# Kernel tuning notes

Measured on AMD Instinct MI355X. Metric: run time of the kernel, lower is better.

## Reference

```python
import jax, jax.numpy as jnp
import numpy as np

N_USERS = 100000
N_ITEMS = 100000
D = 64
B = 2048


def _ancf_layer(q, keys, aW, ab, W1, W2):
    # AttentionMechanism: hidden = relu(keys @ aW.T + ab)  [N, d]
    hidden = jax.nn.relu(keys @ aW.T + ab)
    # scores [B, N]; softmax over keys (dim=1)
    attn = jax.nn.softmax(q @ hidden.T, axis=1)
    q2 = q + attn @ keys  # [B, d]
    # MessageAggregation loop collapsed algebraically:
    # out = W1(q2) + sum_j W1(k_j) + sum_j W2(q2 * k_j)
    #     = W1(q2) + W1(S) + W2(q2 * S),  S = sum_j k_j
    S = keys.sum(axis=0)  # [d]
    out = (q2 + S) @ W1.T + (q2 * S) @ W2.T
    return jax.nn.leaky_relu(out, 0.01)


def setup_inputs() -> dict:
    key = jax.random.key(0)
    ks = jax.random.split(key, 12)
    scale_emb = 0.1
    scale_w = (2.0 / (D + D)) ** 0.5  # xavier-normal std for square layers
    inp = {
        "user_emb": jax.random.normal(ks[0], (N_USERS, D), jnp.float32) * scale_emb,
        "item_emb": jax.random.normal(ks[1], (N_ITEMS, D), jnp.float32) * scale_emb,
        "u_attn_W": jax.random.normal(ks[2], (D, D), jnp.float32) * scale_w,
        "u_attn_b": jnp.zeros((D,), jnp.float32),
        "u_W1": jax.random.normal(ks[3], (D, D), jnp.float32) * scale_w,
        "u_W2": jax.random.normal(ks[4], (D, D), jnp.float32) * scale_w,
        "i_attn_W": jax.random.normal(ks[5], (D, D), jnp.float32) * scale_w,
        "i_attn_b": jnp.zeros((D,), jnp.float32),
        "i_W1": jax.random.normal(ks[6], (D, D), jnp.float32) * scale_w,
        "i_W2": jax.random.normal(ks[7], (D, D), jnp.float32) * scale_w,
        "user_id": jax.random.randint(ks[8], (B,), 0, N_USERS),
        "item_id": jax.random.randint(ks[9], (B,), 0, N_ITEMS),
        "all_user_ids": jnp.arange(N_USERS),
        "all_item_ids": jnp.arange(N_ITEMS),
    }
    return inp


def reference(user_emb, item_emb, u_attn_W, u_attn_b, u_W1, u_W2,
              i_attn_W, i_attn_b, i_W1, i_W2,
              user_id, item_id, all_user_ids, all_item_ids):
    all_user_embeddings = user_emb[all_user_ids]  # [N_users, d]
    all_item_embeddings = item_emb[all_item_ids]  # [N_items, d]
    ue = all_user_embeddings[user_id]  # [B, d]
    ie = all_item_embeddings[item_id]  # [B, d]

    ue_out = _ancf_layer(ue, all_item_embeddings, u_attn_W, u_attn_b, u_W1, u_W2)
    ie_out = _ancf_layer(ie, all_user_embeddings, i_attn_W, i_attn_b, i_W1, i_W2)

    og_user = jnp.concatenate([ue, ue_out], axis=1)  # [B, 2d]
    og_item = jnp.concatenate([ie, ie_out], axis=1)  # [B, 2d]
    return og_user.T @ og_item  # [2d, 2d]
```

## Files before the change

kernel.cpp:

```cpp
#include <hip/hip_runtime.h>


typedef __bf16 bf16x8 __attribute__((ext_vector_type(8)));
typedef float f32x2 __attribute__((ext_vector_type(2)));
typedef float f32x4 __attribute__((ext_vector_type(4)));
typedef float f32x16 __attribute__((ext_vector_type(16)));
typedef unsigned int u32x4 __attribute__((ext_vector_type(4)));
typedef int i32x4 __attribute__((ext_vector_type(4)));
typedef int i32x8 __attribute__((ext_vector_type(8)));

static constexpr int NKEYS  = 100000;
static constexpr int NP     = 101376;
static constexpr int DIM    = 64;
static constexpr int BQ     = 2048;
static constexpr int NCH    = 48;
static constexpr int CHROWS = NP / NCH;
static constexpr int NPH    = CHROWS / 64;
static constexpr int NTIL   = NP / 64;
static constexpr float PADCNT = float(NP - NKEYS);
static constexpr float LOG2E  = 1.44269504088896340736f;

#define DEVINL __device__ __forceinline__

DEVINL unsigned int cvtpk(float lo, float hi) {
    unsigned int r;
    asm("v_cvt_pk_bf16_f32 %0, %1, %2" : "=v"(r) : "v"(lo), "v"(hi));
    return r;
}
DEVINL unsigned short bfr(float f) {
    return (unsigned short)(cvtpk(f, f) & 0xffffu);
}
DEVINL float bf2f(unsigned short u) {
    unsigned int w = (unsigned int)u << 16;
    return __builtin_bit_cast(float, w);
}
DEVINL void permswap(unsigned int& a, unsigned int& b) {
    asm("v_permlane32_swap_b32 %0, %1" : "+v"(a), "+v"(b));
}
DEVINL bf16x8 pack_frag(unsigned int w0, unsigned int w1, unsigned int w2, unsigned int w3) {
    u32x4 t; t[0] = w0; t[1] = w1; t[2] = w2; t[3] = w3;
    return __builtin_bit_cast(bf16x8, t);
}
DEVINL bf16x8 frag8_f32(const float* p) {
    f32x4 a = *reinterpret_cast<const f32x4*>(p);
    f32x4 b = *reinterpret_cast<const f32x4*>(p + 4);
    return pack_frag(cvtpk(a[0], a[1]), cvtpk(a[2], a[3]),
                     cvtpk(b[0], b[1]), cvtpk(b[2], b[3]));
}
DEVINL unsigned int fp8x4(float a, float b, float c, float d) {
    int r = __builtin_amdgcn_cvt_pk_fp8_f32(a, b, 0, false);
    r = __builtin_amdgcn_cvt_pk_fp8_f32(c, d, r, true);
    return (unsigned int)r;
}
DEVINL unsigned char fp8b(float f) {
    return (unsigned char)(__builtin_amdgcn_cvt_pk_fp8_f32(f, f, 0, false) & 0xFF);
}
DEVINL i32x8 ld8(const unsigned char* lo, const unsigned char* hi) {
    union { i32x8 v; i32x4 h[2]; } u;
    u.h[0] = *reinterpret_cast<const i32x4*>(lo);
    u.h[1] = *reinterpret_cast<const i32x4*>(hi);
    return u.v;
}
DEVINL f32x16 mfma8(i32x8 a, i32x8 b, f32x16 c) {
    return __builtin_amdgcn_mfma_scale_f32_32x32x64_f8f6f4(
        a, b, c, 0 , 0 ,
        0, 0x7F7F7F7F, 0, 0x7F7F7F7F);
}
DEVINL float fexp2(float x) {
    float f = __builtin_fmaf(x, 8388608.0f, 1065713994.0f);
    int i = (int)f;
    return __builtin_bit_cast(float, i);
}
DEVINL f32x2 pkadd(f32x2 a, f32x2 b) {
    f32x2 r;
    asm("v_pk_add_f32 %0, %1, %2" : "=v"(r) : "v"(a), "v"(b));
    return r;
}

__global__ __launch_bounds__(256) void prep_kernel(
    const float* __restrict__ user_emb, const float* __restrict__ item_emb,
    const float* __restrict__ uaW, const float* __restrict__ uab,
    const float* __restrict__ iaW, const float* __restrict__ iab,
    unsigned char* __restrict__ Khid, unsigned char* __restrict__ Vpan,
    float* __restrict__ csum)
{
    const int side = blockIdx.y;
    const int tile = blockIdx.x;
    const float* keys = (side == 0) ? item_emb : user_emb;
    const float* aW   = (side == 0) ? uaW : iaW;
    const float* ab   = (side == 0) ? uab : iab;
    unsigned char* Kh  = Khid + (size_t)side * NP * DIM;
    unsigned char* Vps = Vpan + (size_t)side * (NP / 32) * 2048;

    __shared__ float Kf[64][68];
    __shared__ float Wf[64][68];
    __shared__ float bl[64];

    const int t  = threadIdx.x;
    const int r  = t >> 2;
    const int c0 = (t & 3) * 16;

    {
        const float4* src = reinterpret_cast<const float4*>(aW + r * 64 + c0);
        float4* dst = reinterpret_cast<float4*>(&Wf[r][c0]);
        #pragma unroll
        for (int q = 0; q < 4; ++q) dst[q] = src[q];
        if (t < 64) bl[t] = ab[t];
    }
    {
        const int n = tile * 64 + r;
        float4* dst = reinterpret_cast<float4*>(&Kf[r][c0]);
        if (n < NKEYS) {
            const float4* src = reinterpret_cast<const float4*>(keys + (size_t)n * 64 + c0);
            #pragma unroll
            for (int q = 0; q < 4; ++q) dst[q] = src[q];
        } else {
            const float4 z = make_float4(0.f, 0.f, 0.f, 0.f);
            #pragma unroll
            for (int q = 0; q < 4; ++q) dst[q] = z;
        }
    }
    __syncthreads();

    {
        const int wv = t >> 6, lane = t & 63;
        const int c = lane & 31, hi = lane >> 5;
        const int n0 = (wv & 1) * 32, j0 = (wv >> 1) * 32;
        f32x16 acc{};
        #pragma unroll
        for (int ks = 0; ks < 4; ++ks) {
            bf16x8 af = frag8_f32(&Kf[n0 + c][ks * 16 + hi * 8]);
            bf16x8 bf_ = frag8_f32(&Wf[j0 + c][ks * 16 + hi * 8]);
            acc = __builtin_amdgcn_mfma_f32_32x32x16_bf16(af, bf_, acc, 0, 0, 0);
        }
        const float bj = bl[j0 + c];
        #pragma unroll
        for (int rr = 0; rr < 16; ++rr) {
            const int n  = n0 + (rr & 3) + 8 * (rr >> 2) + 4 * hi;
            const int gn = tile * 64 + n;
            float h = fmaxf(acc[rr] + bj, 0.f);
            if (gn >= NKEYS) h = 0.f;
            Kh[(size_t)gn * 64 + j0 + c] = fp8b(h);
        }
    }
    {
        unsigned int pw[4];
        #pragma unroll
        for (int j = 0; j < 4; ++j)
            pw[j] = fp8x4(Kf[c0 + 4 * j][r],     Kf[c0 + 4 * j + 1][r],
                          Kf[c0 + 4 * j + 2][r], Kf[c0 + 4 * j + 3][r]);
        unsigned char* dst = Vps + ((size_t)(2 * tile + (c0 >> 5))) * 2048 + r * 32 + (c0 & 31);
        *reinterpret_cast<uint4*>(dst) = make_uint4(pw[0], pw[1], pw[2], pw[3]);
    }
    if (t < 64) {
        float s = 0.f;
        #pragma unroll 8
        for (int rr = 0; rr < 64; ++rr) s += Kf[rr][t];
        csum[((size_t)side * NTIL + tile) * 64 + t] = s;
    }
}

__global__ __launch_bounds__(64) void sreduceA_kernel(const float* __restrict__ csum,
                                                      float* __restrict__ csum2)
{
    const int j = blockIdx.x, side = blockIdx.y, d = threadIdx.x;
    float s = 0.f;
    for (int idx = j; idx < NTIL; idx += 64)
        s += csum[((size_t)side * NTIL + idx) * 64 + d];
    csum2[((size_t)side * 64 + j) * 64 + d] = s;
}

__global__ __launch_bounds__(64) void sreduceB_kernel(const float* __restrict__ csum2,
                                                      float* __restrict__ Sbuf)
{
    const int side = blockIdx.x, d = threadIdx.x;
    float s = 0.f;
    #pragma unroll 8
    for (int j = 0; j < 64; ++j) s += csum2[((size_t)side * 64 + j) * 64 + d];
    Sbuf[side * 64 + d] = s;
}

__global__ __launch_bounds__(256) void wtrans_kernel(
    const float* __restrict__ uW1, const float* __restrict__ uW2,
    const float* __restrict__ iW1, const float* __restrict__ iW2,
    float* __restrict__ WT)
{
    const float* W = (blockIdx.x == 0) ? uW1 : (blockIdx.x == 1) ? uW2
                   : (blockIdx.x == 2) ? iW1 : iW2;
    float* T = WT + (size_t)blockIdx.x * 4096;
    const int t = threadIdx.x;
    const int j = t >> 2;
    const int dd0 = (t & 3) * 16;
    #pragma unroll
    for (int k = 0; k < 16; ++k)
        T[(dd0 + k) * 64 + j] = W[j * 64 + dd0 + k];
}

__global__ __launch_bounds__(512) void flash_kernel(
    const float* __restrict__ user_emb, const float* __restrict__ item_emb,
    const int* __restrict__ user_id, const int* __restrict__ item_id,
    const unsigned char* __restrict__ Khid, const unsigned char* __restrict__ Vpan,
    unsigned short* __restrict__ Opart, float* __restrict__ lpart)
{
    const int side  = blockIdx.z;
    const int chunk = blockIdx.x;
    const int qblk  = blockIdx.y;
    const int wave  = threadIdx.x >> 6;
    const int lane  = threadIdx.x & 63;
    const int c  = lane & 31;
    const int hi = lane >> 5;

    __shared__ __align__(16) unsigned char KV[3][8192];

    const float* emb = (side == 0) ? user_emb : item_emb;
    const int* ids   = (side == 0) ? user_id  : item_id;
    const unsigned char* Kh = Khid + ((size_t)side * NP + (size_t)chunk * CHROWS) * 64;
    const unsigned char* Vb = Vpan + ((size_t)side * (NP / 32) + (size_t)chunk * (CHROWS / 32)) * 2048;

    const unsigned char* gsrc;
    if (wave < 4) {
        const int st = wave >> 1, qh = wave & 1;
        gsrc = Kh + st * 2048 + qh * 16 + c * 64 + hi * 32;
    } else {
        const int dblk = (wave - 4) >> 1, qh = wave & 1;
        gsrc = Vb + dblk * 1024 + qh * 16 + hi * 2048 + c * 32;
    }

    const unsigned char* gnext = gsrc;
    int ibuf = 0;
    auto ISSUE = [&]() {
        __builtin_amdgcn_global_load_lds(
            (const __attribute__((address_space(1))) unsigned int*)gnext,
            (__attribute__((address_space(3))) unsigned int*)&KV[ibuf][wave * 1024],
            16, 0, 0);
        gnext += 4096;
        ibuf = (ibuf == 2) ? 0 : ibuf + 1;
    };

    ISSUE();
    ISSUE();

    const int qtile = qblk * 256 + wave * 32;
    const int id = ids[qtile + c];
    const float* qrow = emb + (size_t)id * 64 + hi * 32;
    i32x8 bq;
    #pragma unroll
    for (int w = 0; w < 8; ++w) {
        float4 f = *reinterpret_cast<const float4*>(qrow + w * 4);
        bq[w] = (int)fp8x4(f.x * LOG2E, f.y * LOG2E, f.z * LOG2E, f.w * LOG2E);
    }

    f32x16 o0{}, o1{};
    f32x2 lacc0{}, lacc1{};

    asm volatile("s_waitcnt vmcnt(1)" ::: "memory");
    __builtin_amdgcn_s_barrier();

    int cbuf = 0;
    for (int p = 0; p < NPH; ++p) {
        if (p + 2 < NPH) ISSUE();

        const unsigned char* Bp = &KV[cbuf][0];
        cbuf = (cbuf == 2) ? 0 : cbuf + 1;
        const int fo = hi * 512 + c * 16;

        i32x8 ak0 = ld8(Bp + fo,        Bp + 1024 + fo);
        i32x8 ak1 = ld8(Bp + 2048 + fo, Bp + 3072 + fo);

        __builtin_amdgcn_s_setprio(1);
        f32x16 z{};
        f32x16 s0 = mfma8(ak0, bq, z);
        f32x16 s1 = mfma8(ak1, bq, z);
        __builtin_amdgcn_s_setprio(0);

        i32x8 bv0 = ld8(Bp + 4096 + fo, Bp + 5120 + fo);
        i32x8 bv1 = ld8(Bp + 6144 + fo, Bp + 7168 + fo);

        #pragma unroll
        for (int rr = 0; rr < 16; ++rr) s0[rr] = fexp2(s0[rr]);
        #pragma unroll
        for (int rr = 0; rr < 16; ++rr) s1[rr] = fexp2(s1[rr]);

        #pragma unroll
        for (int g = 0; g < 8; ++g) {
            f32x2 a; a[0] = s0[2 * g]; a[1] = s0[2 * g + 1];
            f32x2 b; b[0] = s1[2 * g]; b[1] = s1[2 * g + 1];
            if (g & 1) lacc1 = pkadd(lacc1, pkadd(a, b));
            else       lacc0 = pkadd(lacc0, pkadd(a, b));
        }

        union { i32x8 v; unsigned int w[8]; } pu;
        #pragma unroll
        for (int g = 0; g < 4; ++g) {
            pu.w[2 * g]     = fp8x4(s0[4 * g], s0[4 * g + 1], s0[4 * g + 2], s0[4 * g + 3]);
            pu.w[2 * g + 1] = fp8x4(s1[4 * g], s1[4 * g + 1], s1[4 * g + 2], s1[4 * g + 3]);
            permswap(pu.w[2 * g], pu.w[2 * g + 1]);
        }

        __builtin_amdgcn_s_setprio(1);
        o0 = mfma8(pu.v, bv0, o0);
        o1 = mfma8(pu.v, bv1, o1);
        __builtin_amdgcn_s_setprio(0);

        if (p + 1 < NPH) {
            if (p + 2 < NPH) asm volatile("s_waitcnt vmcnt(1)" ::: "memory");
            else             asm volatile("s_waitcnt vmcnt(0)" ::: "memory");
            __builtin_amdgcn_s_barrier();
        }
    }

    float ls = (lacc0[0] + lacc0[1]) + (lacc1[0] + lacc1[1]);
    ls += __shfl_xor(ls, 32);

    unsigned short* Op = Opart + (((size_t)(side * BQ + qtile)) * NCH + chunk) * 64;
    #pragma unroll
    for (int rr = 0; rr < 16; ++rr) {
        const int q = (rr & 3) + 8 * (rr >> 2) + 4 * hi;
        Op[(size_t)q * NCH * 64 + c]      = bfr(o0[rr]);
        Op[(size_t)q * NCH * 64 + 32 + c] = bfr(o1[rr]);
    }
    if (hi == 0)
        lpart[((size_t)(side * BQ + qtile + c)) * NCH + chunk] = ls;
}

__global__ __launch_bounds__(256) void combine_kernel(
    const float* __restrict__ user_emb, const float* __restrict__ item_emb,
    const int* __restrict__ user_id, const int* __restrict__ item_id,
    const float* __restrict__ WT,
    const unsigned short* __restrict__ Opart, const float* __restrict__ lpart,
    const float* __restrict__ Sbuf,
    float* __restrict__ Aog, float* __restrict__ Bog)
{
    const int bid  = blockIdx.x;
    const int side = bid >> 9;
    const int wave = threadIdx.x >> 6;
    const int lane = threadIdx.x & 63;
    const int q    = ((bid & 511) << 2) + wave;
    const int j    = lane;

    const unsigned short* Ob = Opart + ((size_t)(side * BQ + q)) * (NCH * 64) + j;
    float num = 0.f;
    #pragma unroll 8
    for (int ch = 0; ch < NCH; ++ch)
        num += bf2f(Ob[ch * 64]);

    float lv = (lane < NCH) ? lpart[((size_t)(side * BQ + q)) * NCH + lane] : 0.f;
    #pragma unroll
    for (int m = 32; m >= 1; m >>= 1) lv += __shfl_xor(lv, m);
    const float lsum = lv - PADCNT * fexp2(0.0f);

    const int id = ((side == 0) ? user_id : item_id)[q];
    const float* emb = (side == 0) ? user_emb : item_emb;
    const float e  = emb[(size_t)id * 64 + j];
    const float q2 = e + num / lsum;
    const float Sd = Sbuf[side * 64 + j];

    __shared__ float a1s[4][64], a2s[4][64];
    a1s[wave][j] = q2 + Sd;
    a2s[wave][j] = q2 * Sd;

    const float* W1T = WT + (size_t)side * 8192;
    const float* W2T = W1T + 4096;
    float acc = 0.f;
    #pragma unroll 8
    for (int dd = 0; dd < 64; ++dd)
        acc += a1s[wave][dd] * W1T[dd * 64 + j] + a2s[wave][dd] * W2T[dd * 64 + j];
    const float out = (acc >= 0.f) ? acc : 0.01f * acc;

    float* og = (side == 0) ? Aog : Bog;
    og[(size_t)q * 128 + j]      = e;
    og[(size_t)q * 128 + 64 + j] = out;
}

__global__ __launch_bounds__(256) void final1_kernel(
    const float* __restrict__ Aog, const float* __restrict__ Bog, float* __restrict__ part)
{
    const int b = blockIdx.x;
    const int t = threadIdx.x;
    __shared__ float As[16][128];
    __shared__ float Bs[16][128];
    {
        float* Asf = &As[0][0];
        float* Bsf = &Bs[0][0];
        const float* Ab = Aog + (size_t)b * 16 * 128;
        const float* Bb = Bog + (size_t)b * 16 * 128;
        #pragma unroll
        for (int qq = 0; qq < 2; ++qq) {
            const int off = qq * 1024 + t * 4;
            *reinterpret_cast<float4*>(Asf + off) = *reinterpret_cast<const float4*>(Ab + off);
            *reinterpret_cast<float4*>(Bsf + off) = *reinterpret_cast<const float4*>(Bb + off);
        }
    }
    __syncthreads();

    const int i0 = (t >> 4) * 8, j0 = (t & 15) * 8;
    float acc[8][8] = {};
    #pragma unroll
    for (int k = 0; k < 16; ++k) {
        float av[8], bv[8];
        *reinterpret_cast<f32x4*>(&av[0]) = *reinterpret_cast<const f32x4*>(&As[k][i0]);
        *reinterpret_cast<f32x4*>(&av[4]) = *reinterpret_cast<const f32x4*>(&As[k][i0 + 4]);
        *reinterpret_cast<f32x4*>(&bv[0]) = *reinterpret_cast<const f32x4*>(&Bs[k][j0]);
        *reinterpret_cast<f32x4*>(&bv[4]) = *reinterpret_cast<const f32x4*>(&Bs[k][j0 + 4]);
        #pragma unroll
        for (int ii = 0; ii < 8; ++ii)
            #pragma unroll
            for (int jj = 0; jj < 8; ++jj)
                acc[ii][jj] += av[ii] * bv[jj];
    }
    float* P = part + (size_t)b * 128 * 128;
    #pragma unroll
    for (int ii = 0; ii < 8; ++ii) {
        *reinterpret_cast<float4*>(P + (i0 + ii) * 128 + j0)     = *reinterpret_cast<float4*>(&acc[ii][0]);
        *reinterpret_cast<float4*>(P + (i0 + ii) * 128 + j0 + 4) = *reinterpret_cast<float4*>(&acc[ii][4]);
    }
}

__global__ __launch_bounds__(128) void final2_kernel(const float* __restrict__ part,
                                                     float* __restrict__ out)
{
    const int i = blockIdx.x, j = threadIdx.x;
    float s = 0.f;
    #pragma unroll 8
    for (int b = 0; b < 128; ++b) s += part[(size_t)b * 128 * 128 + i * 128 + j];
    out[i * 128 + j] = s;
}

extern "C" void kernel_launch(void* const* d_in, const int* in_sizes, int n_in,
                              void* d_out, int out_size, void* d_ws, size_t ws_size,
                              hipStream_t stream)
{
    (void)in_sizes; (void)n_in; (void)out_size; (void)ws_size;
    const float* user_emb = (const float*)d_in[0];
    const float* item_emb = (const float*)d_in[1];
    const float* uaW = (const float*)d_in[2];
    const float* uab = (const float*)d_in[3];
    const float* uW1 = (const float*)d_in[4];
    const float* uW2 = (const float*)d_in[5];
    const float* iaW = (const float*)d_in[6];
    const float* iab = (const float*)d_in[7];
    const float* iW1 = (const float*)d_in[8];
    const float* iW2 = (const float*)d_in[9];
    const int* user_id = (const int*)d_in[10];
    const int* item_id = (const int*)d_in[11];

    char* ws = (char*)d_ws;
    size_t off = 0;
    auto alloc = [&](size_t bytes) -> void* {
        void* p = ws + off;
        off = (off + bytes + 255) & ~(size_t)255;
        return p;
    };
    unsigned char* Khid8 = (unsigned char*)alloc((size_t)2 * NP * DIM);
    unsigned char* Vpan8 = (unsigned char*)alloc((size_t)2 * (NP / 32) * 2048);
    float* csum  = (float*)alloc((size_t)2 * NTIL * 64 * 4);
    float* csum2 = (float*)alloc((size_t)2 * 64 * 64 * 4);
    float* Sbuf  = (float*)alloc((size_t)2 * 64 * 4);
    float* WT    = (float*)alloc((size_t)4 * 4096 * 4);
    unsigned short* Opart = (unsigned short*)alloc((size_t)2 * BQ * NCH * 64 * 2);
    float* lpart = (float*)alloc((size_t)2 * BQ * NCH * 4);
    float* Aog   = (float*)alloc((size_t)BQ * 128 * 4);
    float* Bog   = (float*)alloc((size_t)BQ * 128 * 4);
    float* Fpart = (float*)alloc((size_t)128 * 128 * 128 * 4);

    prep_kernel<<<dim3(NTIL, 2), 256, 0, stream>>>(user_emb, item_emb, uaW, uab, iaW, iab,
                                                   Khid8, Vpan8, csum);
    sreduceA_kernel<<<dim3(64, 2), 64, 0, stream>>>(csum, csum2);
    sreduceB_kernel<<<2, 64, 0, stream>>>(csum2, Sbuf);
    wtrans_kernel<<<4, 256, 0, stream>>>(uW1, uW2, iW1, iW2, WT);
    flash_kernel<<<dim3(NCH, BQ / 256, 2), 512, 0, stream>>>(user_emb, item_emb, user_id, item_id,
                                                             Khid8, Vpan8, Opart, lpart);
    combine_kernel<<<2 * BQ / 4, 256, 0, stream>>>(user_emb, item_emb, user_id, item_id,
                                                   WT, Opart, lpart, Sbuf, Aog, Bog);
    final1_kernel<<<128, 256, 0, stream>>>(Aog, Bog, Fpart);
    final2_kernel<<<128, 128, 0, stream>>>(Fpart, (float*)d_out);
}
```

Measured before the change: 127.1 us.

## Load flash K/V operands directly from global memory and merge auxiliary reductions

The flash kernel drops its triple-buffered global-to-LDS staging with barriers. Each wave now loads its K and V fp8 fragments straight from global memory, relying on L1/L2 for reuse, and blocks shrink to 4 waves with twice as many blocks. Separately, the two-stage column-sum reduction and the weight transpose are merged into one small aux kernel, which saves two launches. The change removes barrier and LDS overhead but adds redundant global traffic across waves and loses explicit prefetch overlap.

After: 223.5 us. 1.76x slower.

```diff
diff --git a/kernel.cpp b/kernel.cpp
--- a/kernel.cpp
+++ b/kernel.cpp
@@ -160,87 +160,56 @@
     }
 }
 
-__global__ __launch_bounds__(64) void sreduceA_kernel(const float* __restrict__ csum,
-                                                      float* __restrict__ csum2)
-{
-    const int j = blockIdx.x, side = blockIdx.y, d = threadIdx.x;
-    float s = 0.f;
-    for (int idx = j; idx < NTIL; idx += 64)
-        s += csum[((size_t)side * NTIL + idx) * 64 + d];
-    csum2[((size_t)side * 64 + j) * 64 + d] = s;
-}
-
-__global__ __launch_bounds__(64) void sreduceB_kernel(const float* __restrict__ csum2,
-                                                      float* __restrict__ Sbuf)
-{
-    const int side = blockIdx.x, d = threadIdx.x;
-    float s = 0.f;
-    #pragma unroll 8
-    for (int j = 0; j < 64; ++j) s += csum2[((size_t)side * 64 + j) * 64 + d];
-    Sbuf[side * 64 + d] = s;
-}
-
-__global__ __launch_bounds__(256) void wtrans_kernel(
+__global__ __launch_bounds__(256) void aux_kernel(
+    const float* __restrict__ csum,
     const float* __restrict__ uW1, const float* __restrict__ uW2,
     const float* __restrict__ iW1, const float* __restrict__ iW2,
-    float* __restrict__ WT)
-{
-    const float* W = (blockIdx.x == 0) ? uW1 : (blockIdx.x == 1) ? uW2
-                   : (blockIdx.x == 2) ? iW1 : iW2;
-    float* T = WT + (size_t)blockIdx.x * 4096;
+    float* __restrict__ Sbuf, float* __restrict__ WT)
+{
     const int t = threadIdx.x;
-    const int j = t >> 2;
-    const int dd0 = (t & 3) * 16;
-    #pragma unroll
-    for (int k = 0; k < 16; ++k)
-        T[(dd0 + k) * 64 + j] = W[j * 64 + dd0 + k];
-}
-
-__global__ __launch_bounds__(512) void flash_kernel(
+    if (blockIdx.x < 2) {
+        const int side = blockIdx.x;
+        const int d = t & 63, part = t >> 6;
+        float s = 0.f;
+        for (int idx = part; idx < NTIL; idx += 4)
+            s += csum[((size_t)side * NTIL + idx) * 64 + d];
+        __shared__ float red[4][64];
+        red[part][d] = s;
+        __syncthreads();
+        if (t < 64)
+            Sbuf[side * 64 + t] = red[0][t] + red[1][t] + red[2][t] + red[3][t];
+    } else {
+        const int m = blockIdx.x - 2;
+        const float* W = (m == 0) ? uW1 : (m == 1) ? uW2 : (m == 2) ? iW1 : iW2;
+        float* T = WT + (size_t)m * 4096;
+        const int j = t >> 2;
+        const int dd0 = (t & 3) * 16;
+        #pragma unroll
+        for (int k = 0; k < 16; ++k)
+            T[(dd0 + k) * 64 + j] = W[j * 64 + dd0 + k];
+    }
+}
+
+__global__ __launch_bounds__(256) void flash_kernel(
     const float* __restrict__ user_emb, const float* __restrict__ item_emb,
     const int* __restrict__ user_id, const int* __restrict__ item_id,
     const unsigned char* __restrict__ Khid, const unsigned char* __restrict__ Vpan,
     unsigned short* __restrict__ Opart, float* __restrict__ lpart)
 {
-    const int side  = blockIdx.z;
     const int chunk = blockIdx.x;
     const int qblk  = blockIdx.y;
+    const int side  = blockIdx.z;
     const int wave  = threadIdx.x >> 6;
     const int lane  = threadIdx.x & 63;
     const int c  = lane & 31;
     const int hi = lane >> 5;
 
-    __shared__ __align__(16) unsigned char KV[3][8192];
-
     const float* emb = (side == 0) ? user_emb : item_emb;
     const int* ids   = (side == 0) ? user_id  : item_id;
     const unsigned char* Kh = Khid + ((size_t)side * NP + (size_t)chunk * CHROWS) * 64;
     const unsigned char* Vb = Vpan + ((size_t)side * (NP / 32) + (size_t)chunk * (CHROWS / 32)) * 2048;
 
-    const unsigned char* gsrc;
-    if (wave < 4) {
-        const int st = wave >> 1, qh = wave & 1;
-        gsrc = Kh + st * 2048 + qh * 16 + c * 64 + hi * 32;
-    } else {
-        const int dblk = (wave - 4) >> 1, qh = wave & 1;
-        gsrc = Vb + dblk * 1024 + qh * 16 + hi * 2048 + c * 32;
-    }
-
-    const unsigned char* gnext = gsrc;
-    int ibuf = 0;
-    auto ISSUE = [&]() {
-        __builtin_amdgcn_global_load_lds(
-            (const __attribute__((address_space(1))) unsigned int*)gnext,
-            (__attribute__((address_space(3))) unsigned int*)&KV[ibuf][wave * 1024],
-            16, 0, 0);
-        gnext += 4096;
-        ibuf = (ibuf == 2) ? 0 : ibuf + 1;
-    };
-
-    ISSUE();
-    ISSUE();
-
-    const int qtile = qblk * 256 + wave * 32;
+    const int qtile = qblk * 128 + wave * 32;
     const int id = ids[qtile + c];
     const float* qrow = emb + (size_t)id * 64 + hi * 32;
     i32x8 bq;
@@ -253,19 +222,16 @@
     f32x16 o0{}, o1{};
     f32x2 lacc0{}, lacc1{};
 
-    asm volatile("s_waitcnt vmcnt(1)" ::: "memory");
-    __builtin_amdgcn_s_barrier();
-
-    int cbuf = 0;
+    const unsigned char* Kp = Kh + c * 64 + hi * 32;
+    const unsigned char* Vp = Vb + hi * 2048 + c * 32;
+
     for (int p = 0; p < NPH; ++p) {
-        if (p + 2 < NPH) ISSUE();
-
-        const unsigned char* Bp = &KV[cbuf][0];
-        cbuf = (cbuf == 2) ? 0 : cbuf + 1;
-        const int fo = hi * 512 + c * 16;
-
-        i32x8 ak0 = ld8(Bp + fo,        Bp + 1024 + fo);
-        i32x8 ak1 = ld8(Bp + 2048 + fo, Bp + 3072 + fo);
+        i32x8 ak0 = ld8(Kp,        Kp + 16);
+        i32x8 ak1 = ld8(Kp + 2048, Kp + 2048 + 16);
+        i32x8 bv0 = ld8(Vp,        Vp + 16);
+        i32x8 bv1 = ld8(Vp + 1024, Vp + 1024 + 16);
+        Kp += 4096;
+        Vp += 4096;
 
         __builtin_amdgcn_s_setprio(1);
         f32x16 z{};
@@ -273,9 +239,6 @@
         f32x16 s1 = mfma8(ak1, bq, z);
         __builtin_amdgcn_s_setprio(0);
 
-        i32x8 bv0 = ld8(Bp + 4096 + fo, Bp + 5120 + fo);
-        i32x8 bv1 = ld8(Bp + 6144 + fo, Bp + 7168 + fo);
-
         #pragma unroll
         for (int rr = 0; rr < 16; ++rr) s0[rr] = fexp2(s0[rr]);
         #pragma unroll
@@ -301,12 +264,6 @@
         o0 = mfma8(pu.v, bv0, o0);
         o1 = mfma8(pu.v, bv1, o1);
         __builtin_amdgcn_s_setprio(0);
-
-        if (p + 1 < NPH) {
-            if (p + 2 < NPH) asm volatile("s_waitcnt vmcnt(1)" ::: "memory");
-            else             asm volatile("s_waitcnt vmcnt(0)" ::: "memory");
-            __builtin_amdgcn_s_barrier();
-        }
     }
 
     float ls = (lacc0[0] + lacc0[1]) + (lacc1[0] + lacc1[1]);
@@ -454,7 +411,6 @@
     unsigned char* Khid8 = (unsigned char*)alloc((size_t)2 * NP * DIM);
     unsigned char* Vpan8 = (unsigned char*)alloc((size_t)2 * (NP / 32) * 2048);
     float* csum  = (float*)alloc((size_t)2 * NTIL * 64 * 4);
-    float* csum2 = (float*)alloc((size_t)2 * 64 * 64 * 4);
     float* Sbuf  = (float*)alloc((size_t)2 * 64 * 4);
     float* WT    = (float*)alloc((size_t)4 * 4096 * 4);
     unsigned short* Opart = (unsigned short*)alloc((size_t)2 * BQ * NCH * 64 * 2);
@@ -465,10 +421,8 @@
 
     prep_kernel<<<dim3(NTIL, 2), 256, 0, stream>>>(user_emb, item_emb, uaW, uab, iaW, iab,
                                                    Khid8, Vpan8, csum);
-    sreduceA_kernel<<<dim3(64, 2), 64, 0, stream>>>(csum, csum2);
-    sreduceB_kernel<<<2, 64, 0, stream>>>(csum2, Sbuf);
-    wtrans_kernel<<<4, 256, 0, stream>>>(uW1, uW2, iW1, iW2, WT);
-    flash_kernel<<<dim3(NCH, BQ / 256, 2), 512, 0, stream>>>(user_emb, item_emb, user_id, item_id,
+    aux_kernel<<<6, 256, 0, stream>>>(csum, uW1, uW2, iW1, iW2, Sbuf, WT);
+    flash_kernel<<<dim3(NCH, BQ / 128, 2), 256, 0, stream>>>(user_emb, item_emb, user_id, item_id,
                                                              Khid8, Vpan8, Opart, lpart);
     combine_kernel<<<2 * BQ / 4, 256, 0, stream>>>(user_emb, item_emb, user_id, item_id,
                                                    WT, Opart, lpart, Sbuf, Aog, Bog);
```
